# Performance work log

Measured on AMD Instinct MI355X. Metric: run time of the kernel, lower is better.

Reference implementation:

```python
import jax, jax.numpy as jnp
import numpy as np


def setup_inputs() -> dict:
    key = jax.random.key(0)
    ks = jax.random.split(key, 5)
    b, n, d = 1, 768, 128
    scale = 1.0 / np.sqrt(d)
    x = jax.random.normal(ks[0], (b, n, d), dtype=jnp.float32)
    W_in = jax.random.normal(ks[1], (d, d), dtype=jnp.float32) * scale
    b_in = jax.random.normal(ks[2], (d,), dtype=jnp.float32) * 0.02
    W_out = jax.random.normal(ks[3], (d, d), dtype=jnp.float32) * scale
    b_out = jax.random.normal(ks[4], (d,), dtype=jnp.float32) * 0.02
    return {"x": x, "W_in": W_in, "b_in": b_in, "W_out": W_out, "b_out": b_out}


def reference(x, W_in, b_in, W_out, b_out):
    # proj_in applied to x (original calls it twice on the same input; identical result)
    left = jnp.einsum('bid,ed->bie', x, W_in) + b_in          # [b, n, d]
    # broadcast outer product: [b, i, 1, d] * [b, 1, j, d] -> [b, i, j, d]
    outer = left[:, :, None, :] * left[:, None, :, :]
    # proj_out over feature dim
    out = jnp.einsum('bijd,ed->bije', outer, W_out) + b_out    # [b, n, n, d]
    return out
```

## Files before the change

### kernel.cpp

```cpp
#include <hip/hip_runtime.h>

#define Nn 768
#define Dd 128
#define LDP 136

typedef __attribute__((ext_vector_type(8))) short bf16x8;
typedef __attribute__((ext_vector_type(4))) float f32x4;
typedef __attribute__((ext_vector_type(4))) int   i32x4;

static __device__ __forceinline__ unsigned short f2bf(float f) {
  unsigned int u = __builtin_bit_cast(unsigned int, f);
  u += 0x7fffu + ((u >> 16) & 1u);
  return (unsigned short)(u >> 16);
}
static __device__ __forceinline__ float bf2f(unsigned short h) {
  unsigned int u = ((unsigned int)h) << 16;
  return __builtin_bit_cast(float, u);
}
static __device__ __forceinline__ unsigned int cvtpk(float lo, float hi) {
  unsigned int r;
  asm("v_cvt_pk_bf16_f32 %0, %1, %2" : "=v"(r) : "v"(lo), "v"(hi));
  return r;
}

__global__ __launch_bounds__(128)
void k_left(const float* __restrict__ x, const float* __restrict__ Win,
            const float* __restrict__ bin, unsigned short* __restrict__ left) {
  __shared__ float sx[Dd];
  const int i = blockIdx.x;
  const int e = threadIdx.x;
  sx[e] = x[i * Dd + e];
  __syncthreads();
  const float4* wrow = (const float4*)(Win + e * Dd);
  float a0 = 0.f, a1 = 0.f, a2 = 0.f, a3 = 0.f;
#pragma unroll
  for (int d4 = 0; d4 < Dd / 4; d4 += 4) {
    float4 w0 = wrow[d4+0], w1 = wrow[d4+1], w2 = wrow[d4+2], w3 = wrow[d4+3];
    a0 += sx[4*d4+ 0]*w0.x + sx[4*d4+ 1]*w0.y + sx[4*d4+ 2]*w0.z + sx[4*d4+ 3]*w0.w;
    a1 += sx[4*d4+ 4]*w1.x + sx[4*d4+ 5]*w1.y + sx[4*d4+ 6]*w1.z + sx[4*d4+ 7]*w1.w;
    a2 += sx[4*d4+ 8]*w2.x + sx[4*d4+ 9]*w2.y + sx[4*d4+10]*w2.z + sx[4*d4+11]*w2.w;
    a3 += sx[4*d4+12]*w3.x + sx[4*d4+13]*w3.y + sx[4*d4+14]*w3.z + sx[4*d4+15]*w3.w;
  }
  left[i * Dd + e] = f2bf(((a0 + a1) + (a2 + a3)) + bin[e]);
}

__global__ __launch_bounds__(512, 6)
void k_outer(const unsigned short* __restrict__ left, const float* __restrict__ Wout,
             const float* __restrict__ bout, float* __restrict__ out) {
  __shared__ __attribute__((aligned(16))) unsigned short sB[128 * LDP];
  __shared__ float sLi[Dd];
  __shared__ float sBo[Dd];

  const int jt = blockIdx.x;
  const int i  = blockIdx.y;
  const int t  = threadIdx.x;

  if (t < Dd) {
    sLi[t] = bf2f(left[i * Dd + t]);
    sBo[t] = bout[t];
  }
  __syncthreads();

  {
    const int row = t >> 4;
    const int c8  = (t & 15) * 8;
    float l[8];
#pragma unroll
    for (int q = 0; q < 8; ++q) l[q] = sLi[c8 + q];
#pragma unroll
    for (int it = 0; it < 4; ++it) {
      const int r = row + it * 32;
      const float4* wp = (const float4*)(Wout + r * Dd + c8);
      float4 w0 = wp[0], w1 = wp[1];
      i32x4 vb;
      vb[0] = (int)cvtpk(w0.x * l[0], w0.y * l[1]);
      vb[1] = (int)cvtpk(w0.z * l[2], w0.w * l[3]);
      vb[2] = (int)cvtpk(w1.x * l[4], w1.y * l[5]);
      vb[3] = (int)cvtpk(w1.z * l[6], w1.w * l[7]);
      *(i32x4*)(sB + r * LDP + c8) = vb;
    }
  }
  __syncthreads();

  const int wid  = t >> 6;
  const int lane = t & 63;
  const int l15  = lane & 15;
  const int kq   = (lane >> 4) * 8;

  float bias[8];
#pragma unroll
  for (int n = 0; n < 8; ++n) bias[n] = sBo[n * 16 + l15];

  const unsigned short* gA = left + (size_t)(jt * 128 + wid * 16 + l15) * Dd;
  bf16x8 A[4];
#pragma unroll
  for (int kb = 0; kb < 4; ++kb) A[kb] = *(const bf16x8*)(gA + kb * 32 + kq);

  f32x4 acc[8] = {};
#pragma unroll
  for (int n = 0; n < 8; ++n) {
    const unsigned short* sBrow = sB + (n * 16 + l15) * LDP + kq;
#pragma unroll
    for (int kb = 0; kb < 4; ++kb) {
      bf16x8 b = *(const bf16x8*)(sBrow + kb * 32);
      acc[n] = __builtin_amdgcn_mfma_f32_16x16x32_bf16(A[kb], b, acc[n], 0, 0, 0);
    }
  }

#pragma unroll
  for (int r = 0; r < 4; ++r) {
    const int j = jt * 128 + wid * 16 + (lane >> 4) * 4 + r;
    float* orow = out + ((size_t)i * Nn + j) * Dd;
#pragma unroll
    for (int n = 0; n < 8; ++n) {
      orow[n * 16 + l15] = acc[n][r] + bias[n];
    }
  }
}

extern "C" void kernel_launch(void* const* d_in, const int* in_sizes, int n_in,
                              void* d_out, int out_size, void* d_ws, size_t ws_size,
                              hipStream_t stream) {
  const float* x    = (const float*)d_in[0];
  const float* Win  = (const float*)d_in[1];
  const float* bin  = (const float*)d_in[2];
  const float* Wout = (const float*)d_in[3];
  const float* bout = (const float*)d_in[4];
  float* out = (float*)d_out;
  unsigned short* left = (unsigned short*)d_ws;

  k_left<<<Nn, Dd, 0, stream>>>(x, Win, bin, left);
  dim3 grid(Nn / 128, Nn);
  k_outer<<<grid, 512, 0, stream>>>(left, Wout, bout, out);
}
```

Measured before the change: 63.68 us.

## Process two i rows per block to reuse A fragments and Wout loads

Each k_outer block now handles two output rows i instead of one. It builds two scaled-Wout B tiles in LDS from a single Wout load and reuses the register-held A fragments for both. The A global loads are hoisted before the first barrier so they overlap with the LDS fill. This halves the grid and the per-output Wout reads and conversions. In exchange, LDS use doubles and the occupancy hint drops from 6 to 4 blocks per CU, which may reduce latency hiding for the output stores that dominate.

```diff
diff --git a/kernel.cpp b/kernel.cpp
--- a/kernel.cpp
+++ b/kernel.cpp
@@ -44,76 +44,88 @@
   left[i * Dd + e] = f2bf(((a0 + a1) + (a2 + a3)) + bin[e]);
 }
 
-__global__ __launch_bounds__(512, 6)
+__global__ __launch_bounds__(512, 4)
 void k_outer(const unsigned short* __restrict__ left, const float* __restrict__ Wout,
              const float* __restrict__ bout, float* __restrict__ out) {
-  __shared__ __attribute__((aligned(16))) unsigned short sB[128 * LDP];
-  __shared__ float sLi[Dd];
+  __shared__ __attribute__((aligned(16))) unsigned short sB[2][128 * LDP];
+  __shared__ float sLi[2][Dd];
   __shared__ float sBo[Dd];
 
   const int jt = blockIdx.x;
-  const int i  = blockIdx.y;
+  const int ip = blockIdx.y;
   const int t  = threadIdx.x;
 
-  if (t < Dd) {
-    sLi[t] = bf2f(left[i * Dd + t]);
-    sBo[t] = bout[t];
+  if (t < 256) {
+    const int h = t >> 7, e = t & 127;
+    sLi[h][e] = bf2f(left[(ip * 2 + h) * Dd + e]);
+    if (h == 0) sBo[e] = bout[e];
   }
+
+  const int wid  = t >> 6;
+  const int lane = t & 63;
+  const int l15  = lane & 15;
+  const int kq   = (lane >> 4) * 8;
+
+  const unsigned short* gA = left + (size_t)(jt * 128 + wid * 16 + l15) * Dd;
+  bf16x8 A[4];
+#pragma unroll
+  for (int kb = 0; kb < 4; ++kb) A[kb] = *(const bf16x8*)(gA + kb * 32 + kq);
+
   __syncthreads();
 
   {
     const int row = t >> 4;
     const int c8  = (t & 15) * 8;
-    float l[8];
+    float l0[8], l1[8];
 #pragma unroll
-    for (int q = 0; q < 8; ++q) l[q] = sLi[c8 + q];
+    for (int q = 0; q < 8; ++q) { l0[q] = sLi[0][c8 + q]; l1[q] = sLi[1][c8 + q]; }
 #pragma unroll
     for (int it = 0; it < 4; ++it) {
       const int r = row + it * 32;
       const float4* wp = (const float4*)(Wout + r * Dd + c8);
       float4 w0 = wp[0], w1 = wp[1];
       i32x4 vb;
-      vb[0] = (int)cvtpk(w0.x * l[0], w0.y * l[1]);
-      vb[1] = (int)cvtpk(w0.z * l[2], w0.w * l[3]);
-      vb[2] = (int)cvtpk(w1.x * l[4], w1.y * l[5]);
-      vb[3] = (int)cvtpk(w1.z * l[6], w1.w * l[7]);
-      *(i32x4*)(sB + r * LDP + c8) = vb;
+      vb[0] = (int)cvtpk(w0.x * l0[0], w0.y * l0[1]);
+      vb[1] = (int)cvtpk(w0.z * l0[2], w0.w * l0[3]);
+      vb[2] = (int)cvtpk(w1.x * l0[4], w1.y * l0[5]);
+      vb[3] = (int)cvtpk(w1.z * l0[6], w1.w * l0[7]);
+      *(i32x4*)(&sB[0][0] + r * LDP + c8) = vb;
+      vb[0] = (int)cvtpk(w0.x * l1[0], w0.y * l1[1]);
+      vb[1] = (int)cvtpk(w0.z * l1[2], w0.w * l1[3]);
+      vb[2] = (int)cvtpk(w1.x * l1[4], w1.y * l1[5]);
+      vb[3] = (int)cvtpk(w1.z * l1[6], w1.w * l1[7]);
+      *(i32x4*)(&sB[1][0] + r * LDP + c8) = vb;
     }
   }
   __syncthreads();
-
-  const int wid  = t >> 6;
-  const int lane = t & 63;
-  const int l15  = lane & 15;
-  const int kq   = (lane >> 4) * 8;
 
   float bias[8];
 #pragma unroll
   for (int n = 0; n < 8; ++n) bias[n] = sBo[n * 16 + l15];
 
-  const unsigned short* gA = left + (size_t)(jt * 128 + wid * 16 + l15) * Dd;
-  bf16x8 A[4];
 #pragma unroll
-  for (int kb = 0; kb < 4; ++kb) A[kb] = *(const bf16x8*)(gA + kb * 32 + kq);
+  for (int h = 0; h < 2; ++h) {
+    const int i = ip * 2 + h;
 
-  f32x4 acc[8] = {};
+    f32x4 acc[8] = {};
 #pragma unroll
-  for (int n = 0; n < 8; ++n) {
-    const unsigned short* sBrow = sB + (n * 16 + l15) * LDP + kq;
+    for (int n = 0; n < 8; ++n) {
+      const unsigned short* sBrow = &sB[h][0] + (n * 16 + l15) * LDP + kq;
 #pragma unroll
-    for (int kb = 0; kb < 4; ++kb) {
-      bf16x8 b = *(const bf16x8*)(sBrow + kb * 32);
-      acc[n] = __builtin_amdgcn_mfma_f32_16x16x32_bf16(A[kb], b, acc[n], 0, 0, 0);
+      for (int kb = 0; kb < 4; ++kb) {
+        bf16x8 b = *(const bf16x8*)(sBrow + kb * 32);
+        acc[n] = __builtin_amdgcn_mfma_f32_16x16x32_bf16(A[kb], b, acc[n], 0, 0, 0);
+      }
     }
-  }
 
 #pragma unroll
-  for (int r = 0; r < 4; ++r) {
-    const int j = jt * 128 + wid * 16 + (lane >> 4) * 4 + r;
-    float* orow = out + ((size_t)i * Nn + j) * Dd;
+    for (int r = 0; r < 4; ++r) {
+      const int j = jt * 128 + wid * 16 + (lane >> 4) * 4 + r;
+      float* orow = out + ((size_t)i * Nn + j) * Dd;
 #pragma unroll
-    for (int n = 0; n < 8; ++n) {
-      orow[n * 16 + l15] = acc[n][r] + bias[n];
+      for (int n = 0; n < 8; ++n) {
+        orow[n * 16 + l15] = acc[n][r] + bias[n];
+      }
     }
   }
 }
@@ -130,6 +142,6 @@
   unsigned short* left = (unsigned short*)d_ws;
 
   k_left<<<Nn, Dd, 0, stream>>>(x, Win, bin, left);
-  dim3 grid(Nn / 128, Nn);
+  dim3 grid(Nn / 128, Nn / 2);
   k_outer<<<grid, 512, 0, stream>>>(left, Wout, bout, out);
 }
```

New measurement: 68.63 us. +7.8%, slower.
